# Performance work log

Measured on AMD Instinct MI355X. Metric: run time of the kernel, lower is better.

The kernel has to match this reference:

```python
import jax, jax.numpy as jnp
import numpy as np

D_MODEL = 256
N_HEADS = 8
D_K = D_MODEL // N_HEADS
N = 4096
N_SEG = 16


def setup_inputs() -> dict:
    key = jax.random.key(0)
    ks = jax.random.split(key, 12)
    s = 0.02
    x_q = jax.random.normal(ks[0], (N, D_MODEL), jnp.float32)
    x_kv = jax.random.normal(ks[1], (N, D_MODEL), jnp.float32)
    # same key -> identical segment ids so every query segment exists in kv
    batch = jnp.sort(jax.random.randint(ks[2], (N,), 0, N_SEG)).astype(jnp.int64)
    params = {}
    names = ['Wq', 'Wk', 'Wv', 'Wo']
    for i, n in enumerate(names):
        params[n] = jax.random.normal(ks[3 + i], (D_MODEL, D_MODEL), jnp.float32) * s
        params['b' + n[1]] = jnp.zeros((D_MODEL,), jnp.float32)
    return dict(x_q=x_q, x_kv=x_kv, batch_q=batch, batch_kv=batch, **params)


def reference(x_q, x_kv, batch_q, batch_kv, Wq, bq, Wk, bk, Wv, bv, Wo, bo):
    # projections (torch Linear: x @ W.T + b)
    q = (x_q @ Wq.T + bq).reshape(N, N_HEADS, D_K)   # [Nq, H, dk]
    k = (x_kv @ Wk.T + bk).reshape(N, N_HEADS, D_K)  # [Nkv, H, dk]
    v = (x_kv @ Wv.T + bv).reshape(N, N_HEADS, D_K)
    scores = jnp.einsum('qhd,khd->hqk', q, k) / jnp.sqrt(jnp.float32(D_K))
    mask = batch_q[:, None] == batch_kv[None, :]      # block-diagonal [Nq, Nkv]
    scores = jnp.where(mask[None], scores, -jnp.inf)
    attn = jax.nn.softmax(scores, axis=-1)            # [H, Nq, Nkv]
    out = jnp.einsum('hqk,khd->qhd', attn, v).reshape(N, D_MODEL)
    out = out @ Wo.T + bo
    return out, attn[None]  # match torch's [1, H, Nq, Nkv] attn shape
```

## Files before the change

### kernel.cpp

```cpp
#include <hip/hip_runtime.h>

#define N_TOK 4096
#define DM 256
#define NH 8
#define DK 32

using u16 = unsigned short;
using u32 = unsigned int;
using i64 = long long;
typedef float f32x4 __attribute__((ext_vector_type(4)));

__device__ __forceinline__ float bf2f(u16 u){ return __uint_as_float(((u32)u) << 16); }
__device__ __forceinline__ u16 f2bf(float f){
    u32 x = __float_as_uint(f);
    x += 0x7fffu + ((x >> 16) & 1u);
    return (u16)(x >> 16);
}

__global__ __launch_bounds__(256)
void bounds_kernel(const void* __restrict__ batch_q, const void* __restrict__ batch_kv,
                   int2* __restrict__ bounds)
{
    int q = blockIdx.x * 256 + threadIdx.x;
    const int* kv32 = (const int*)batch_kv;
    const i64* kv64 = (const i64*)batch_kv;
    bool is64 = (kv32[N_TOK - 1] == 0);
    int s = is64 ? (int)((const i64*)batch_q)[q] : ((const int*)batch_q)[q];
    int lo = 0, hi = N_TOK;
    while (lo < hi){ int m = (lo + hi) >> 1; int v = is64 ? (int)kv64[m] : kv32[m]; if (v < s) lo = m + 1; else hi = m; }
    int lo2 = lo, hi2 = N_TOK;
    while (lo2 < hi2){ int m = (lo2 + hi2) >> 1; int v = is64 ? (int)kv64[m] : kv32[m]; if (v <= s) lo2 = m + 1; else hi2 = m; }
    bounds[q] = make_int2(lo, lo2);
}

template<int OUT_BF16>
__global__ __launch_bounds__(256)
void proj_kernel(const float* __restrict__ x, const float* __restrict__ W,
                 const float* __restrict__ bias, void* __restrict__ outv)
{
    const int ROWS = 16;
    int row0 = blockIdx.x * ROWS;
    int c = threadIdx.x;
    float acc[ROWS];
    float bv = bias[c];
#pragma unroll
    for (int r = 0; r < ROWS; ++r) acc[r] = bv;

    const float4* Wv = (const float4*)(W + (size_t)c * DM);
    for (int i = 0; i < DM / 4; ++i){
        float4 w = Wv[i];
        int d0 = i * 4;
#pragma unroll
        for (int r = 0; r < ROWS; ++r){
            const float* xr = x + (size_t)(row0 + r) * DM + d0;
            acc[r] += xr[0] * w.x + xr[1] * w.y + xr[2] * w.z + xr[3] * w.w;
        }
    }
#pragma unroll
    for (int r = 0; r < ROWS; ++r){
        size_t idx = (size_t)(row0 + r) * DM + c;
        if (OUT_BF16) ((u16*)outv)[idx] = f2bf(acc[r]);
        else          ((float*)outv)[idx] = acc[r];
    }
}

__global__ __launch_bounds__(256)
void proj_kv_kernel(const float* __restrict__ x, const float* __restrict__ Wk,
                    const float* __restrict__ bk, const float* __restrict__ Wv,
                    const float* __restrict__ bv, u16* __restrict__ Kp,
                    u16* __restrict__ Vp)
{
    const int ROWS = 16;
    int row0 = blockIdx.x * ROWS;
    int c = threadIdx.x;
    float acck[ROWS], accv[ROWS];
    float bkv = bk[c], bvv = bv[c];
#pragma unroll
    for (int r = 0; r < ROWS; ++r){ acck[r] = bkv; accv[r] = bvv; }

    const float4* Wk4 = (const float4*)(Wk + (size_t)c * DM);
    const float4* Wv4 = (const float4*)(Wv + (size_t)c * DM);
    for (int i = 0; i < DM / 4; ++i){
        float4 wk = Wk4[i];
        float4 wv = Wv4[i];
        int d0 = i * 4;
#pragma unroll
        for (int r = 0; r < ROWS; ++r){
            const float* xr = x + (size_t)(row0 + r) * DM + d0;
            float x0 = xr[0], x1 = xr[1], x2 = xr[2], x3 = xr[3];
            acck[r] += x0 * wk.x + x1 * wk.y + x2 * wk.z + x3 * wk.w;
            accv[r] += x0 * wv.x + x1 * wv.y + x2 * wv.z + x3 * wv.w;
        }
    }
#pragma unroll
    for (int r = 0; r < ROWS; ++r){
        size_t idx = (size_t)(row0 + r) * DM + c;
        Kp[idx] = f2bf(acck[r]);
        Vp[idx] = f2bf(accv[r]);
    }
}

__global__ __launch_bounds__(256)
void attn_kernel(const float* __restrict__ Q, const u16* __restrict__ K,
                 const u16* __restrict__ V, const int2* __restrict__ bounds,
                 float* __restrict__ attn, float* __restrict__ O)
{
    __shared__ float sc[N_TOK];
    __shared__ float qs[DK];
    __shared__ float red[8];
    __shared__ float Osh[DK];

    int q = blockIdx.x, h = blockIdx.y, tid = threadIdx.x;
    int2 bnd = bounds[q];
    const int lo = bnd.x, hi = bnd.y;

    if (tid < DK){ qs[tid] = Q[(size_t)q * DM + h * DK + tid]; Osh[tid] = 0.f; }
    __syncthreads();

    const float scale = 0.17677669529663687f;

    float lmax = -1e30f;
    for (int k = lo + tid; k < hi; k += 256){
        const uint4* kr = (const uint4*)(K + (size_t)k * DM + h * DK);
        float dot = 0.f;
#pragma unroll
        for (int i = 0; i < 4; ++i){
            uint4 p = kr[i];
            dot += qs[i*8+0]*bf2f((u16)p.x) + qs[i*8+1]*bf2f((u16)(p.x>>16));
            dot += qs[i*8+2]*bf2f((u16)p.y) + qs[i*8+3]*bf2f((u16)(p.y>>16));
            dot += qs[i*8+4]*bf2f((u16)p.z) + qs[i*8+5]*bf2f((u16)(p.z>>16));
            dot += qs[i*8+6]*bf2f((u16)p.w) + qs[i*8+7]*bf2f((u16)(p.w>>16));
        }
        dot *= scale;
        sc[k - lo] = dot;
        lmax = fmaxf(lmax, dot);
    }
#pragma unroll
    for (int off = 32; off; off >>= 1) lmax = fmaxf(lmax, __shfl_xor(lmax, off, 64));
    if ((tid & 63) == 0) red[tid >> 6] = lmax;
    __syncthreads();
    float m = fmaxf(fmaxf(red[0], red[1]), fmaxf(red[2], red[3]));

    float lsum = 0.f;
    for (int k = lo + tid; k < hi; k += 256){
        float p = __expf(sc[k - lo] - m);
        sc[k - lo] = p;
        lsum += p;
    }
#pragma unroll
    for (int off = 32; off; off >>= 1) lsum += __shfl_xor(lsum, off, 64);
    if ((tid & 63) == 0) red[4 + (tid >> 6)] = lsum;
    __syncthreads();
    float sum = red[4] + red[5] + red[6] + red[7];
    float inv = (sum > 0.f) ? (1.0f / sum) : 0.f;

    int d2 = tid & 15;
    int g  = tid >> 4;
    float p0 = 0.f, p1 = 0.f;
    for (int k = lo + g; k < hi; k += 16){
        u32 pv = *(const u32*)(V + (size_t)k * DM + h * DK + 2 * d2);
        float p = sc[k - lo];
        p0 += p * bf2f((u16)pv);
        p1 += p * bf2f((u16)(pv >> 16));
    }
    p0 += __shfl_xor(p0, 16, 64); p0 += __shfl_xor(p0, 32, 64);
    p1 += __shfl_xor(p1, 16, 64); p1 += __shfl_xor(p1, 32, 64);
    if ((tid & 63) < 16){
        atomicAdd(&Osh[2 * d2 + 0], p0);
        atomicAdd(&Osh[2 * d2 + 1], p1);
    }

    f32x4* arow4 = (f32x4*)(attn + ((size_t)h * N_TOK + q) * N_TOK);
#pragma unroll
    for (int i = 0; i < N_TOK / 1024; ++i){
        int t = i * 256 + tid;
        int k0 = 4 * t;
        f32x4 w;
        w.x = (k0 + 0 >= lo && k0 + 0 < hi) ? sc[k0 + 0 - lo] * inv : 0.f;
        w.y = (k0 + 1 >= lo && k0 + 1 < hi) ? sc[k0 + 1 - lo] * inv : 0.f;
        w.z = (k0 + 2 >= lo && k0 + 2 < hi) ? sc[k0 + 2 - lo] * inv : 0.f;
        w.w = (k0 + 3 >= lo && k0 + 3 < hi) ? sc[k0 + 3 - lo] * inv : 0.f;
        __builtin_nontemporal_store(w, &arow4[t]);
    }

    __syncthreads();
    if (tid < DK) O[(size_t)q * DM + h * DK + tid] = Osh[tid] * inv;
}

extern "C" void kernel_launch(void* const* d_in, const int* in_sizes, int n_in,
                              void* d_out, int out_size, void* d_ws, size_t ws_size,
                              hipStream_t stream)
{
    const float* x_q  = (const float*)d_in[0];
    const float* x_kv = (const float*)d_in[1];
    const void* batch_q  = d_in[2];
    const void* batch_kv = d_in[3];
    const float* Wq = (const float*)d_in[4];
    const float* bq = (const float*)d_in[5];
    const float* Wk = (const float*)d_in[6];
    const float* bk = (const float*)d_in[7];
    const float* Wv = (const float*)d_in[8];
    const float* bv = (const float*)d_in[9];
    const float* Wo = (const float*)d_in[10];
    const float* bo = (const float*)d_in[11];

    char* ws = (char*)d_ws;
    float* Q  = (float*)ws;
    u16*   Kp = (u16*)(ws + (size_t)4 * 1024 * 1024);
    u16*   Vp = (u16*)(ws + (size_t)6 * 1024 * 1024);
    float* O  = (float*)(ws + (size_t)8 * 1024 * 1024);
    int2* bounds = (int2*)(ws + (size_t)12 * 1024 * 1024);

    float* out  = (float*)d_out;
    float* attn = out + (size_t)N_TOK * DM;

    bounds_kernel<<<N_TOK / 256, 256, 0, stream>>>(batch_q, batch_kv, bounds);
    proj_kernel<0><<<N_TOK/16, 256, 0, stream>>>(x_q,  Wq, bq, Q);
    proj_kv_kernel<<<N_TOK/16, 256, 0, stream>>>(x_kv, Wk, bk, Wv, bv, Kp, Vp);
    attn_kernel<<<dim3(N_TOK, NH), 256, 0, stream>>>(Q, Kp, Vp, bounds, attn, O);
    proj_kernel<0><<<N_TOK/16, 256, 0, stream>>>((const float*)O, Wo, bo, out);
}
```

Baseline: 715.6 us.

## Fuse all heads per query into one block with per-head 32-lane online softmax

The attention kernel now launches one block per query instead of one per (query, head). Each group of 32 threads handles one head, keeping q in registers and using an online max/sum in a single pass over K with shuffle reductions, which removes the block-wide syncs and LDS atomics. The attention row is written as scalar stores for the segment plus vectorised zero fills elsewhere. Segments longer than 768 fall back to a sequential per-head loop, and only 32 threads per head means less parallelism per head and scalar, less-coalesced stores in the segment region.

```diff
diff --git a/kernel.cpp b/kernel.cpp
--- a/kernel.cpp
+++ b/kernel.cpp
@@ -4,6 +4,7 @@
 #define DM 256
 #define NH 8
 #define DK 32
+#define SEGMAX 768
 
 using u16 = unsigned short;
 using u32 = unsigned int;
@@ -45,7 +46,6 @@
     float bv = bias[c];
 #pragma unroll
     for (int r = 0; r < ROWS; ++r) acc[r] = bv;
-
     const float4* Wv = (const float4*)(W + (size_t)c * DM);
     for (int i = 0; i < DM / 4; ++i){
         float4 w = Wv[i];
@@ -77,7 +77,6 @@
     float bkv = bk[c], bvv = bv[c];
 #pragma unroll
     for (int r = 0; r < ROWS; ++r){ acck[r] = bkv; accv[r] = bvv; }
-
     const float4* Wk4 = (const float4*)(Wk + (size_t)c * DM);
     const float4* Wv4 = (const float4*)(Wv + (size_t)c * DM);
     for (int i = 0; i < DM / 4; ++i){
@@ -101,90 +100,154 @@
 }
 
 __global__ __launch_bounds__(256)
-void attn_kernel(const float* __restrict__ Q, const u16* __restrict__ K,
-                 const u16* __restrict__ V, const int2* __restrict__ bounds,
-                 float* __restrict__ attn, float* __restrict__ O)
-{
-    __shared__ float sc[N_TOK];
-    __shared__ float qs[DK];
+void attn_fused(const float* __restrict__ Q, const u16* __restrict__ K,
+                const u16* __restrict__ V, const int2* __restrict__ bounds,
+                float* __restrict__ attn, float* __restrict__ O)
+{
+    __shared__ float sc[NH][SEGMAX];
     __shared__ float red[8];
     __shared__ float Osh[DK];
 
-    int q = blockIdx.x, h = blockIdx.y, tid = threadIdx.x;
-    int2 bnd = bounds[q];
-    const int lo = bnd.x, hi = bnd.y;
-
-    if (tid < DK){ qs[tid] = Q[(size_t)q * DM + h * DK + tid]; Osh[tid] = 0.f; }
-    __syncthreads();
-
+    int q = blockIdx.x, tid = threadIdx.x;
+    int2 b = bounds[q];
+    const int lo = b.x, hi = b.y, seg = hi - lo;
     const float scale = 0.17677669529663687f;
 
-    float lmax = -1e30f;
-    for (int k = lo + tid; k < hi; k += 256){
-        const uint4* kr = (const uint4*)(K + (size_t)k * DM + h * DK);
-        float dot = 0.f;
-#pragma unroll
-        for (int i = 0; i < 4; ++i){
-            uint4 p = kr[i];
-            dot += qs[i*8+0]*bf2f((u16)p.x) + qs[i*8+1]*bf2f((u16)(p.x>>16));
-            dot += qs[i*8+2]*bf2f((u16)p.y) + qs[i*8+3]*bf2f((u16)(p.y>>16));
-            dot += qs[i*8+4]*bf2f((u16)p.z) + qs[i*8+5]*bf2f((u16)(p.z>>16));
-            dot += qs[i*8+6]*bf2f((u16)p.w) + qs[i*8+7]*bf2f((u16)(p.w>>16));
-        }
-        dot *= scale;
-        sc[k - lo] = dot;
-        lmax = fmaxf(lmax, dot);
-    }
-#pragma unroll
-    for (int off = 32; off; off >>= 1) lmax = fmaxf(lmax, __shfl_xor(lmax, off, 64));
-    if ((tid & 63) == 0) red[tid >> 6] = lmax;
-    __syncthreads();
-    float m = fmaxf(fmaxf(red[0], red[1]), fmaxf(red[2], red[3]));
-
-    float lsum = 0.f;
-    for (int k = lo + tid; k < hi; k += 256){
-        float p = __expf(sc[k - lo] - m);
-        sc[k - lo] = p;
-        lsum += p;
-    }
-#pragma unroll
-    for (int off = 32; off; off >>= 1) lsum += __shfl_xor(lsum, off, 64);
-    if ((tid & 63) == 0) red[4 + (tid >> 6)] = lsum;
-    __syncthreads();
-    float sum = red[4] + red[5] + red[6] + red[7];
-    float inv = (sum > 0.f) ? (1.0f / sum) : 0.f;
-
-    int d2 = tid & 15;
-    int g  = tid >> 4;
-    float p0 = 0.f, p1 = 0.f;
-    for (int k = lo + g; k < hi; k += 16){
-        u32 pv = *(const u32*)(V + (size_t)k * DM + h * DK + 2 * d2);
-        float p = sc[k - lo];
-        p0 += p * bf2f((u16)pv);
-        p1 += p * bf2f((u16)(pv >> 16));
-    }
-    p0 += __shfl_xor(p0, 16, 64); p0 += __shfl_xor(p0, 32, 64);
-    p1 += __shfl_xor(p1, 16, 64); p1 += __shfl_xor(p1, 32, 64);
-    if ((tid & 63) < 16){
-        atomicAdd(&Osh[2 * d2 + 0], p0);
-        atomicAdd(&Osh[2 * d2 + 1], p1);
-    }
-
-    f32x4* arow4 = (f32x4*)(attn + ((size_t)h * N_TOK + q) * N_TOK);
-#pragma unroll
-    for (int i = 0; i < N_TOK / 1024; ++i){
-        int t = i * 256 + tid;
-        int k0 = 4 * t;
-        f32x4 w;
-        w.x = (k0 + 0 >= lo && k0 + 0 < hi) ? sc[k0 + 0 - lo] * inv : 0.f;
-        w.y = (k0 + 1 >= lo && k0 + 1 < hi) ? sc[k0 + 1 - lo] * inv : 0.f;
-        w.z = (k0 + 2 >= lo && k0 + 2 < hi) ? sc[k0 + 2 - lo] * inv : 0.f;
-        w.w = (k0 + 3 >= lo && k0 + 3 < hi) ? sc[k0 + 3 - lo] * inv : 0.f;
-        __builtin_nontemporal_store(w, &arow4[t]);
-    }
-
-    __syncthreads();
-    if (tid < DK) O[(size_t)q * DM + h * DK + tid] = Osh[tid] * inv;
+    if (seg <= SEGMAX){
+        int h = tid >> 5, j = tid & 31;
+        float qf[32];
+        const float4* qp = (const float4*)(Q + (size_t)q * DM + h * DK);
+#pragma unroll
+        for (int i = 0; i < 8; ++i){
+            float4 v = qp[i];
+            qf[4*i] = v.x; qf[4*i+1] = v.y; qf[4*i+2] = v.z; qf[4*i+3] = v.w;
+        }
+        float m = -1e30f, l = 0.f;
+        for (int k = lo + j; k < hi; k += 32){
+            const uint4* kr = (const uint4*)(K + (size_t)k * DM + h * DK);
+            float dot = 0.f;
+#pragma unroll
+            for (int i = 0; i < 4; ++i){
+                uint4 p = kr[i];
+                dot += qf[i*8+0]*bf2f((u16)p.x) + qf[i*8+1]*bf2f((u16)(p.x>>16));
+                dot += qf[i*8+2]*bf2f((u16)p.y) + qf[i*8+3]*bf2f((u16)(p.y>>16));
+                dot += qf[i*8+4]*bf2f((u16)p.z) + qf[i*8+5]*bf2f((u16)(p.z>>16));
+                dot += qf[i*8+6]*bf2f((u16)p.w) + qf[i*8+7]*bf2f((u16)(p.w>>16));
+            }
+            dot *= scale;
+            sc[h][k - lo] = dot;
+            float nm = fmaxf(m, dot);
+            l = l * __expf(m - nm) + __expf(dot - nm);
+            m = nm;
+        }
+#pragma unroll
+        for (int off = 16; off; off >>= 1){
+            float mo = __shfl_xor(m, off, 64);
+            float lx = __shfl_xor(l, off, 64);
+            float nm = fmaxf(m, mo);
+            l = l * __expf(m - nm) + lx * __expf(mo - nm);
+            m = nm;
+        }
+        float inv = (l > 0.f) ? (1.f / l) : 0.f;
+
+        float* arow = attn + ((size_t)h * N_TOK + q) * N_TOK;
+        for (int k = lo + j; k < hi; k += 32){
+            float p = __expf(sc[h][k - lo] - m) * inv;
+            sc[h][k - lo] = p;
+            __builtin_nontemporal_store(p, &arow[k]);
+        }
+        int lo4 = lo & ~3, hi4 = (hi + 3) & ~3;
+        f32x4 z4 = {0.f, 0.f, 0.f, 0.f};
+        for (int t = j; t < (lo4 >> 2); t += 32)
+            __builtin_nontemporal_store(z4, (f32x4*)arow + t);
+        for (int k = lo4 + j; k < lo; k += 32)
+            __builtin_nontemporal_store(0.f, &arow[k]);
+        for (int k = hi + j; k < hi4; k += 32)
+            __builtin_nontemporal_store(0.f, &arow[k]);
+        for (int t = (hi4 >> 2) + j; t < N_TOK / 4; t += 32)
+            __builtin_nontemporal_store(z4, (f32x4*)arow + t);
+
+        int d2 = j & 15, g = j >> 4;
+        float p0 = 0.f, p1 = 0.f;
+        for (int k = lo + g; k < hi; k += 2){
+            u32 pv = *(const u32*)(V + (size_t)k * DM + h * DK + 2 * d2);
+            float p = sc[h][k - lo];
+            p0 += p * bf2f((u16)pv);
+            p1 += p * bf2f((u16)(pv >> 16));
+        }
+        p0 += __shfl_xor(p0, 16, 64);
+        p1 += __shfl_xor(p1, 16, 64);
+        if (g == 0){
+            float2 o2 = make_float2(p0, p1);
+            *(float2*)(O + (size_t)q * DM + h * DK + 2 * d2) = o2;
+        }
+    } else {
+        float* scf = &sc[0][0];
+        for (int h = 0; h < NH; ++h){
+            const float* qrow = Q + (size_t)q * DM + h * DK;
+            float lmax = -1e30f;
+            for (int k = lo + tid; k < hi; k += 256){
+                const uint4* kr = (const uint4*)(K + (size_t)k * DM + h * DK);
+                float dot = 0.f;
+#pragma unroll
+                for (int i = 0; i < 4; ++i){
+                    uint4 p = kr[i];
+                    dot += qrow[i*8+0]*bf2f((u16)p.x) + qrow[i*8+1]*bf2f((u16)(p.x>>16));
+                    dot += qrow[i*8+2]*bf2f((u16)p.y) + qrow[i*8+3]*bf2f((u16)(p.y>>16));
+                    dot += qrow[i*8+4]*bf2f((u16)p.z) + qrow[i*8+5]*bf2f((u16)(p.z>>16));
+                    dot += qrow[i*8+6]*bf2f((u16)p.w) + qrow[i*8+7]*bf2f((u16)(p.w>>16));
+                }
+                dot *= scale;
+                scf[k - lo] = dot;
+                lmax = fmaxf(lmax, dot);
+            }
+#pragma unroll
+            for (int off = 32; off; off >>= 1) lmax = fmaxf(lmax, __shfl_xor(lmax, off, 64));
+            if ((tid & 63) == 0) red[tid >> 6] = lmax;
+            __syncthreads();
+            float mm = fmaxf(fmaxf(red[0], red[1]), fmaxf(red[2], red[3]));
+            float lsum = 0.f;
+            for (int k = lo + tid; k < hi; k += 256){
+                float p = __expf(scf[k - lo] - mm);
+                scf[k - lo] = p;
+                lsum += p;
+            }
+#pragma unroll
+            for (int off = 32; off; off >>= 1) lsum += __shfl_xor(lsum, off, 64);
+            if ((tid & 63) == 0) red[4 + (tid >> 6)] = lsum;
+            if (tid < DK) Osh[tid] = 0.f;
+            __syncthreads();
+            float s = red[4] + red[5] + red[6] + red[7];
+            float inv = (s > 0.f) ? (1.f / s) : 0.f;
+            float* arow = attn + ((size_t)h * N_TOK + q) * N_TOK;
+            for (int t = tid; t < N_TOK / 4; t += 256){
+                int k0 = 4 * t;
+                f32x4 w;
+                w.x = (k0+0 >= lo && k0+0 < hi) ? scf[k0+0-lo]*inv : 0.f;
+                w.y = (k0+1 >= lo && k0+1 < hi) ? scf[k0+1-lo]*inv : 0.f;
+                w.z = (k0+2 >= lo && k0+2 < hi) ? scf[k0+2-lo]*inv : 0.f;
+                w.w = (k0+3 >= lo && k0+3 < hi) ? scf[k0+3-lo]*inv : 0.f;
+                __builtin_nontemporal_store(w, (f32x4*)arow + t);
+            }
+            int d2 = tid & 15, g = tid >> 4;
+            float p0 = 0.f, p1 = 0.f;
+            for (int k = lo + g; k < hi; k += 16){
+                u32 pv = *(const u32*)(V + (size_t)k * DM + h * DK + 2 * d2);
+                float p = scf[k - lo];
+                p0 += p * bf2f((u16)pv);
+                p1 += p * bf2f((u16)(pv >> 16));
+            }
+            p0 += __shfl_xor(p0, 16, 64); p0 += __shfl_xor(p0, 32, 64);
+            p1 += __shfl_xor(p1, 16, 64); p1 += __shfl_xor(p1, 32, 64);
+            if ((tid & 63) < 16){
+                atomicAdd(&Osh[2*d2 + 0], p0);
+                atomicAdd(&Osh[2*d2 + 1], p1);
+            }
+            __syncthreads();
+            if (tid < DK) O[(size_t)q * DM + h * DK + tid] = Osh[tid] * inv;
+            __syncthreads();
+        }
+    }
 }
 
 extern "C" void kernel_launch(void* const* d_in, const int* in_sizes, int n_in,
@@ -217,6 +280,6 @@
     bounds_kernel<<<N_TOK / 256, 256, 0, stream>>>(batch_q, batch_kv, bounds);
     proj_kernel<0><<<N_TOK/16, 256, 0, stream>>>(x_q,  Wq, bq, Q);
     proj_kv_kernel<<<N_TOK/16, 256, 0, stream>>>(x_kv, Wk, bk, Wv, bv, Kp, Vp);
-    attn_kernel<<<dim3(N_TOK, NH), 256, 0, stream>>>(Q, Kp, Vp, bounds, attn, O);
+    attn_fused<<<N_TOK, 256, 0, stream>>>(Q, Kp, Vp, bounds, attn, O);
     proj_kernel<0><<<N_TOK/16, 256, 0, stream>>>((const float*)O, Wo, bo, out);
 }
```

Result: slower. 788.1 us (+10.1%).

## Tile attention over 8 queries per block with head-major K/V layout

Applied to the files above, without the earlier changes.

K and V are now stored head-major so each head's keys are contiguous. The attention kernel processes 8 consecutive queries per block, with each wave handling two queries over the shared key span of the tile. It uses an online max/sum softmax and skips explicit work on the zero regions beyond plain stores. A fallback path handles tiles whose span exceeds a shared-memory cap. The goal is fewer blocks, K/V loads reused across queries, and fewer barriers, at the cost of computing masked scores across the union span and more register pressure.

```diff
diff --git a/kernel.cpp b/kernel.cpp
--- a/kernel.cpp
+++ b/kernel.cpp
@@ -4,6 +4,7 @@
 #define DM 256
 #define NH 8
 #define DK 32
+#define SPANMAX 768
 
 using u16 = unsigned short;
 using u32 = unsigned int;
@@ -45,7 +46,6 @@
     float bv = bias[c];
 #pragma unroll
     for (int r = 0; r < ROWS; ++r) acc[r] = bv;
-
     const float4* Wv = (const float4*)(W + (size_t)c * DM);
     for (int i = 0; i < DM / 4; ++i){
         float4 w = Wv[i];
@@ -73,11 +73,11 @@
     const int ROWS = 16;
     int row0 = blockIdx.x * ROWS;
     int c = threadIdx.x;
+    int hh = c >> 5, dd = c & 31;
     float acck[ROWS], accv[ROWS];
     float bkv = bk[c], bvv = bv[c];
 #pragma unroll
     for (int r = 0; r < ROWS; ++r){ acck[r] = bkv; accv[r] = bvv; }
-
     const float4* Wk4 = (const float4*)(Wk + (size_t)c * DM);
     const float4* Wv4 = (const float4*)(Wv + (size_t)c * DM);
     for (int i = 0; i < DM / 4; ++i){
@@ -94,97 +94,207 @@
     }
 #pragma unroll
     for (int r = 0; r < ROWS; ++r){
-        size_t idx = (size_t)(row0 + r) * DM + c;
+        size_t idx = ((size_t)hh * N_TOK + (row0 + r)) * DK + dd;
         Kp[idx] = f2bf(acck[r]);
         Vp[idx] = f2bf(accv[r]);
     }
 }
 
 __global__ __launch_bounds__(256)
-void attn_kernel(const float* __restrict__ Q, const u16* __restrict__ K,
-                 const u16* __restrict__ V, const int2* __restrict__ bounds,
-                 float* __restrict__ attn, float* __restrict__ O)
-{
-    __shared__ float sc[N_TOK];
-    __shared__ float qs[DK];
-    __shared__ float red[8];
-    __shared__ float Osh[DK];
-
-    int q = blockIdx.x, h = blockIdx.y, tid = threadIdx.x;
-    int2 bnd = bounds[q];
-    const int lo = bnd.x, hi = bnd.y;
-
-    if (tid < DK){ qs[tid] = Q[(size_t)q * DM + h * DK + tid]; Osh[tid] = 0.f; }
-    __syncthreads();
-
+void attn_fused(const float* __restrict__ Q, const u16* __restrict__ K,
+                const u16* __restrict__ V, const int2* __restrict__ bounds,
+                float* __restrict__ attn, float* __restrict__ O)
+{
+    __shared__ float sc[NH][SPANMAX];
+    __shared__ float red[4][2];
+    __shared__ float osh[DK];
+
+    int tile = blockIdx.x, h = blockIdx.y, tid = threadIdx.x;
+    int qbase = tile * 8;
+    int klo = bounds[qbase].x;
+    int khi = bounds[qbase + 7].y;
+    int span = khi - klo;
+    const u16* Kh = K + (size_t)h * N_TOK * DK;
+    const u16* Vh = V + (size_t)h * N_TOK * DK;
     const float scale = 0.17677669529663687f;
 
-    float lmax = -1e30f;
-    for (int k = lo + tid; k < hi; k += 256){
-        const uint4* kr = (const uint4*)(K + (size_t)k * DM + h * DK);
-        float dot = 0.f;
-#pragma unroll
-        for (int i = 0; i < 4; ++i){
-            uint4 p = kr[i];
-            dot += qs[i*8+0]*bf2f((u16)p.x) + qs[i*8+1]*bf2f((u16)(p.x>>16));
-            dot += qs[i*8+2]*bf2f((u16)p.y) + qs[i*8+3]*bf2f((u16)(p.y>>16));
-            dot += qs[i*8+4]*bf2f((u16)p.z) + qs[i*8+5]*bf2f((u16)(p.z>>16));
-            dot += qs[i*8+6]*bf2f((u16)p.w) + qs[i*8+7]*bf2f((u16)(p.w>>16));
-        }
-        dot *= scale;
-        sc[k - lo] = dot;
-        lmax = fmaxf(lmax, dot);
-    }
-#pragma unroll
-    for (int off = 32; off; off >>= 1) lmax = fmaxf(lmax, __shfl_xor(lmax, off, 64));
-    if ((tid & 63) == 0) red[tid >> 6] = lmax;
-    __syncthreads();
-    float m = fmaxf(fmaxf(red[0], red[1]), fmaxf(red[2], red[3]));
-
-    float lsum = 0.f;
-    for (int k = lo + tid; k < hi; k += 256){
-        float p = __expf(sc[k - lo] - m);
-        sc[k - lo] = p;
-        lsum += p;
-    }
-#pragma unroll
-    for (int off = 32; off; off >>= 1) lsum += __shfl_xor(lsum, off, 64);
-    if ((tid & 63) == 0) red[4 + (tid >> 6)] = lsum;
-    __syncthreads();
-    float sum = red[4] + red[5] + red[6] + red[7];
-    float inv = (sum > 0.f) ? (1.0f / sum) : 0.f;
-
-    int d2 = tid & 15;
-    int g  = tid >> 4;
-    float p0 = 0.f, p1 = 0.f;
-    for (int k = lo + g; k < hi; k += 16){
-        u32 pv = *(const u32*)(V + (size_t)k * DM + h * DK + 2 * d2);
-        float p = sc[k - lo];
-        p0 += p * bf2f((u16)pv);
-        p1 += p * bf2f((u16)(pv >> 16));
-    }
-    p0 += __shfl_xor(p0, 16, 64); p0 += __shfl_xor(p0, 32, 64);
-    p1 += __shfl_xor(p1, 16, 64); p1 += __shfl_xor(p1, 32, 64);
-    if ((tid & 63) < 16){
-        atomicAdd(&Osh[2 * d2 + 0], p0);
-        atomicAdd(&Osh[2 * d2 + 1], p1);
-    }
-
-    f32x4* arow4 = (f32x4*)(attn + ((size_t)h * N_TOK + q) * N_TOK);
-#pragma unroll
-    for (int i = 0; i < N_TOK / 1024; ++i){
-        int t = i * 256 + tid;
-        int k0 = 4 * t;
-        f32x4 w;
-        w.x = (k0 + 0 >= lo && k0 + 0 < hi) ? sc[k0 + 0 - lo] * inv : 0.f;
-        w.y = (k0 + 1 >= lo && k0 + 1 < hi) ? sc[k0 + 1 - lo] * inv : 0.f;
-        w.z = (k0 + 2 >= lo && k0 + 2 < hi) ? sc[k0 + 2 - lo] * inv : 0.f;
-        w.w = (k0 + 3 >= lo && k0 + 3 < hi) ? sc[k0 + 3 - lo] * inv : 0.f;
-        __builtin_nontemporal_store(w, &arow4[t]);
-    }
-
-    __syncthreads();
-    if (tid < DK) O[(size_t)q * DM + h * DK + tid] = Osh[tid] * inv;
+    if (span <= SPANMAX){
+        int w = tid >> 6, lane = tid & 63;
+        int q0 = qbase + 2 * w;
+        int2 b0 = bounds[q0], b1 = bounds[q0 + 1];
+        float q0f[32], q1f[32];
+        {
+            const float4* qp0 = (const float4*)(Q + (size_t)q0 * DM + h * DK);
+            const float4* qp1 = (const float4*)(Q + (size_t)(q0 + 1) * DM + h * DK);
+#pragma unroll
+            for (int i = 0; i < 8; ++i){
+                float4 a = qp0[i], b = qp1[i];
+                q0f[4*i]=a.x; q0f[4*i+1]=a.y; q0f[4*i+2]=a.z; q0f[4*i+3]=a.w;
+                q1f[4*i]=b.x; q1f[4*i+1]=b.y; q1f[4*i+2]=b.z; q1f[4*i+3]=b.w;
+            }
+        }
+        float m0 = -1e30f, l0 = 0.f, m1 = -1e30f, l1 = 0.f;
+        for (int k = klo + lane; k < khi; k += 64){
+            const uint4* kr = (const uint4*)(Kh + (size_t)k * DK);
+            float d0 = 0.f, d1 = 0.f;
+#pragma unroll
+            for (int i = 0; i < 4; ++i){
+                uint4 pp = kr[i];
+                float f;
+                f = bf2f((u16)pp.x);        d0 += q0f[8*i+0]*f; d1 += q1f[8*i+0]*f;
+                f = bf2f((u16)(pp.x>>16));  d0 += q0f[8*i+1]*f; d1 += q1f[8*i+1]*f;
+                f = bf2f((u16)pp.y);        d0 += q0f[8*i+2]*f; d1 += q1f[8*i+2]*f;
+                f = bf2f((u16)(pp.y>>16));  d0 += q0f[8*i+3]*f; d1 += q1f[8*i+3]*f;
+                f = bf2f((u16)pp.z);        d0 += q0f[8*i+4]*f; d1 += q1f[8*i+4]*f;
+                f = bf2f((u16)(pp.z>>16));  d0 += q0f[8*i+5]*f; d1 += q1f[8*i+5]*f;
+                f = bf2f((u16)pp.w);        d0 += q0f[8*i+6]*f; d1 += q1f[8*i+6]*f;
+                f = bf2f((u16)(pp.w>>16));  d0 += q0f[8*i+7]*f; d1 += q1f[8*i+7]*f;
+            }
+            d0 = (k >= b0.x && k < b0.y) ? d0 * scale : -1e30f;
+            d1 = (k >= b1.x && k < b1.y) ? d1 * scale : -1e30f;
+            sc[2*w  ][k - klo] = d0;
+            sc[2*w+1][k - klo] = d1;
+            float nm = fmaxf(m0, d0);
+            l0 = l0 * __expf(m0 - nm) + __expf(d0 - nm); m0 = nm;
+            nm = fmaxf(m1, d1);
+            l1 = l1 * __expf(m1 - nm) + __expf(d1 - nm); m1 = nm;
+        }
+#pragma unroll
+        for (int off = 32; off; off >>= 1){
+            float mo = __shfl_xor(m0, off, 64), lx = __shfl_xor(l0, off, 64);
+            float nm = fmaxf(m0, mo);
+            l0 = l0 * __expf(m0 - nm) + lx * __expf(mo - nm); m0 = nm;
+            mo = __shfl_xor(m1, off, 64); lx = __shfl_xor(l1, off, 64);
+            nm = fmaxf(m1, mo);
+            l1 = l1 * __expf(m1 - nm) + lx * __expf(mo - nm); m1 = nm;
+        }
+        float inv0 = (l0 > 0.f) ? (1.f / l0) : 0.f;
+        float inv1 = (l1 > 0.f) ? (1.f / l1) : 0.f;
+
+        int tql = klo >> 2, tqh = (khi + 3) >> 2;
+        f32x4 z4 = {0.f, 0.f, 0.f, 0.f};
+#pragma unroll
+        for (int r = 0; r < 2; ++r){
+            float mq  = r ? m1 : m0;
+            float invq = r ? inv1 : inv0;
+            float* srow = sc[2*w + r];
+            f32x4* arow4 = (f32x4*)(attn + ((size_t)h * N_TOK + (q0 + r)) * N_TOK);
+            for (int t = lane; t < tql; t += 64)
+                __builtin_nontemporal_store(z4, arow4 + t);
+            for (int t = tqh + lane; t < N_TOK / 4; t += 64)
+                __builtin_nontemporal_store(z4, arow4 + t);
+            for (int t = tql + lane; t < tqh; t += 64){
+                int k0 = 4 * t;
+                f32x4 vq;
+#pragma unroll
+                for (int e = 0; e < 4; ++e){
+                    int k = k0 + e;
+                    bool in = (k >= klo && k < khi);
+                    int idx = k - klo; idx = idx < 0 ? 0 : (idx >= SPANMAX ? SPANMAX - 1 : idx);
+                    float p = in ? __expf(srow[idx] - mq) * invq : 0.f;
+                    if (in) srow[idx] = p;
+                    vq[e] = p;
+                }
+                __builtin_nontemporal_store(vq, arow4 + t);
+            }
+        }
+
+        int d2 = lane & 15, par = (lane >> 4) & 1, qq = lane >> 5;
+        float* srow = sc[2*w + qq];
+        float a0 = 0.f, a1 = 0.f;
+        for (int k = klo + par; k < khi; k += 2){
+            u32 pv = *(const u32*)(Vh + (size_t)k * DK + 2 * d2);
+            float p = srow[k - klo];
+            a0 += p * bf2f((u16)pv);
+            a1 += p * bf2f((u16)(pv >> 16));
+        }
+        a0 += __shfl_xor(a0, 16, 64);
+        a1 += __shfl_xor(a1, 16, 64);
+        if (par == 0)
+            *(float2*)(O + (size_t)(q0 + qq) * DM + h * DK + 2 * d2) = make_float2(a0, a1);
+    } else {
+        float* scf = &sc[0][0];
+        for (int qi = 0; qi < 8; ++qi){
+            int qg = qbase + qi;
+            int2 bq = bounds[qg];
+            int lo = bq.x, hi = bq.y;
+            float qf[32];
+            const float4* qp = (const float4*)(Q + (size_t)qg * DM + h * DK);
+#pragma unroll
+            for (int i = 0; i < 8; ++i){
+                float4 v = qp[i];
+                qf[4*i]=v.x; qf[4*i+1]=v.y; qf[4*i+2]=v.z; qf[4*i+3]=v.w;
+            }
+            float m = -1e30f, l = 0.f;
+            for (int k = lo + tid; k < hi; k += 256){
+                const uint4* kr = (const uint4*)(Kh + (size_t)k * DK);
+                float dot = 0.f;
+#pragma unroll
+                for (int i = 0; i < 4; ++i){
+                    uint4 pp = kr[i];
+                    dot += qf[8*i+0]*bf2f((u16)pp.x) + qf[8*i+1]*bf2f((u16)(pp.x>>16));
+                    dot += qf[8*i+2]*bf2f((u16)pp.y) + qf[8*i+3]*bf2f((u16)(pp.y>>16));
+                    dot += qf[8*i+4]*bf2f((u16)pp.z) + qf[8*i+5]*bf2f((u16)(pp.z>>16));
+                    dot += qf[8*i+6]*bf2f((u16)pp.w) + qf[8*i+7]*bf2f((u16)(pp.w>>16));
+                }
+                dot *= scale;
+                float nm = fmaxf(m, dot);
+                l = l * __expf(m - nm) + __expf(dot - nm); m = nm;
+            }
+#pragma unroll
+            for (int off = 32; off; off >>= 1){
+                float mo = __shfl_xor(m, off, 64), lx = __shfl_xor(l, off, 64);
+                float nm = fmaxf(m, mo);
+                l = l * __expf(m - nm) + lx * __expf(mo - nm); m = nm;
+            }
+            if ((tid & 63) == 0){ red[tid >> 6][0] = m; red[tid >> 6][1] = l; }
+            if (tid < DK) osh[tid] = 0.f;
+            __syncthreads();
+            float fm = -1e30f, fl = 0.f;
+#pragma unroll
+            for (int i2 = 0; i2 < 4; ++i2){
+                float mo = red[i2][0], lx = red[i2][1];
+                float nm = fmaxf(fm, mo);
+                fl = fl * __expf(fm - nm) + lx * __expf(mo - nm); fm = nm;
+            }
+            float inv = (fl > 0.f) ? (1.f / fl) : 0.f;
+            float* arow = attn + ((size_t)h * N_TOK + qg) * N_TOK;
+            for (int k = lo + tid; k < hi; k += 256){
+                const uint4* kr = (const uint4*)(Kh + (size_t)k * DK);
+                float dot = 0.f;
+#pragma unroll
+                for (int i = 0; i < 4; ++i){
+                    uint4 pp = kr[i];
+                    dot += qf[8*i+0]*bf2f((u16)pp.x) + qf[8*i+1]*bf2f((u16)(pp.x>>16));
+                    dot += qf[8*i+2]*bf2f((u16)pp.y) + qf[8*i+3]*bf2f((u16)(pp.y>>16));
+                    dot += qf[8*i+4]*bf2f((u16)pp.z) + qf[8*i+5]*bf2f((u16)(pp.z>>16));
+                    dot += qf[8*i+6]*bf2f((u16)pp.w) + qf[8*i+7]*bf2f((u16)(pp.w>>16));
+                }
+                float p = __expf(dot * scale - fm) * inv;
+                scf[k - lo] = p;
+                __builtin_nontemporal_store(p, &arow[k]);
+            }
+            int tql = lo >> 2, tqh2 = (hi + 3) >> 2;
+            f32x4 z4 = {0.f, 0.f, 0.f, 0.f};
+            for (int t = tid; t < tql; t += 256)
+                __builtin_nontemporal_store(z4, (f32x4*)arow + t);
+            for (int t = tqh2 + tid; t < N_TOK / 4; t += 256)
+                __builtin_nontemporal_store(z4, (f32x4*)arow + t);
+            for (int k = 4 * tql + tid; k < lo; k += 256)
+                __builtin_nontemporal_store(0.f, &arow[k]);
+            for (int k = hi + tid; k < 4 * tqh2; k += 256)
+                __builtin_nontemporal_store(0.f, &arow[k]);
+            __syncthreads();
+            int d = tid & 31, grp = tid >> 5;
+            float acc = 0.f;
+            for (int k = lo + grp; k < hi; k += 8)
+                acc += scf[k - lo] * bf2f(Vh[(size_t)k * DK + d]);
+            atomicAdd(&osh[d], acc);
+            __syncthreads();
+            if (tid < DK) O[(size_t)qg * DM + h * DK + tid] = osh[tid];
+            __syncthreads();
+        }
+    }
 }
 
 extern "C" void kernel_launch(void* const* d_in, const int* in_sizes, int n_in,
@@ -217,6 +327,6 @@
     bounds_kernel<<<N_TOK / 256, 256, 0, stream>>>(batch_q, batch_kv, bounds);
     proj_kernel<0><<<N_TOK/16, 256, 0, stream>>>(x_q,  Wq, bq, Q);
     proj_kv_kernel<<<N_TOK/16, 256, 0, stream>>>(x_kv, Wk, bk, Wv, bv, Kp, Vp);
-    attn_kernel<<<dim3(N_TOK, NH), 256, 0, stream>>>(Q, Kp, Vp, bounds, attn, O);
+    attn_fused<<<dim3(N_TOK/8, NH), 256, 0, stream>>>(Q, Kp, Vp, bounds, attn, O);
     proj_kernel<0><<<N_TOK/16, 256, 0, stream>>>((const float*)O, Wo, bo, out);
 }
```

Result: slower. 815.2 us (+13.9%).
